# Performance work log

Measured on AMD Instinct MI355X. Metric: run time of the kernel, lower is better.

Reference implementation:

```python
import jax, jax.numpy as jnp
import numpy as np

N, E, D, H = 20000, 320000, 128, 256
NUM_FINE = 2


def _mlp(x, W1, b1, W2, b2):
    # Linear -> relu -> Linear -> relu (dropout rate 0.0 is identity)
    h = jax.nn.relu(x @ W1 + b1)
    return jax.nn.relu(h @ W2 + b2)


def setup_inputs() -> dict:
    key = jax.random.key(0)
    ks = jax.random.split(key, 12)

    def p(k, shape):
        fan_in = shape[0]
        return jax.random.normal(k, shape, jnp.float32) * (1.0 / fan_in) ** 0.5

    return {
        "nodes": jax.random.normal(ks[0], (N, D), jnp.float32),
        "edges": jax.random.normal(ks[1], (E, D), jnp.float32),
        "senders": jax.random.randint(ks[2], (E,), 0, N, jnp.int32),
        "receivers": jax.random.randint(ks[3], (E,), 0, N, jnp.int32),
        # embed node MLP: D -> H -> D
        "Wn1": p(ks[4], (D, H)), "bn1": jnp.zeros((H,), jnp.float32),
        "Wn2": p(ks[5], (H, D)), "bn2": jnp.zeros((D,), jnp.float32),
        # embed edge MLP: D -> H -> D
        "We1": p(ks[6], (D, H)), "be1": jnp.zeros((H,), jnp.float32),
        "We2": p(ks[7], (H, D)), "be2": jnp.zeros((D,), jnp.float32),
        # edge model MLP: 3D -> H -> D  (concat[src, dest, edge_attr])
        "Wed1": p(ks[8], (3 * D, H)), "bed1": jnp.zeros((H,), jnp.float32),
        "Wed2": p(ks[9], (H, D)), "bed2": jnp.zeros((D,), jnp.float32),
        # node model MLP: 2D -> H -> D  (concat[x, segment_sum(edge_attr)])
        "Wnd1": p(ks[10], (2 * D, H)), "bnd1": jnp.zeros((H,), jnp.float32),
        "Wnd2": p(ks[11], (H, D)), "bnd2": jnp.zeros((D,), jnp.float32),
    }


def reference(nodes, edges, senders, receivers,
              Wn1, bn1, Wn2, bn2, We1, be1, We2, be2,
              Wed1, bed1, Wed2, bed2, Wnd1, bnd1, Wnd2, bnd2):
    # Embed stage (EmbedMetaLayer)
    x = _mlp(nodes, Wn1, bn1, Wn2, bn2)   # (N, D)
    e = _mlp(edges, We1, be1, We2, be2)   # (E, D)

    pooled = []
    for _ in range(NUM_FINE):
        # EdgeModel: gather src/dest node feats, concat with edge feats, MLP
        edge_in = jnp.concatenate([x[senders], x[receivers], e], axis=-1)  # (E, 3D)
        e = _mlp(edge_in, Wed1, bed1, Wed2, bed2)                           # (E, D)
        # NodeModel: scatter-add edge feats to receiver nodes, concat, MLP
        agg = jax.ops.segment_sum(e, receivers, num_segments=N)            # (N, D)
        x = _mlp(jnp.concatenate([x, agg], axis=-1), Wnd1, bnd1, Wnd2, bnd2)  # (N, D)
        # global_add_pooling: vmap(jnp.sum) over nodes -> per-node feature sum (N,)
        pooled.append(jnp.sum(x, axis=-1))
    # concatenate along last axis of the 1-D pooled vectors -> (NUM_FINE * N,)
    return jnp.concatenate(pooled, axis=-1)
```

## Files before the change

### kernel.cpp

```cpp
#include <hip/hip_runtime.h>
#include <stdint.h>

#define N_NODES 20000
#define N_EDGES 320000

typedef __attribute__((ext_vector_type(8)))  __bf16        bf16x8;
typedef __attribute__((ext_vector_type(16))) float         f32x16;
typedef __attribute__((ext_vector_type(4)))  float         f32x4v;
typedef __attribute__((ext_vector_type(4)))  uint32_t      u32x4;
typedef __attribute__((ext_vector_type(8)))  unsigned short us8;
typedef __attribute__((ext_vector_type(2)))  unsigned short us2;

static __device__ __forceinline__ unsigned short cvt_bf16(float f) {
  uint32_t u = __builtin_bit_cast(uint32_t, f);
  u = (u + 0x7fffu + ((u >> 16) & 1u)) >> 16;
  return (unsigned short)u;
}
static __device__ __forceinline__ float cvt_f32(unsigned short h) {
  uint32_t u = ((uint32_t)h) << 16;
  return __builtin_bit_cast(float, u);
}

static __device__ __forceinline__ void gll16(const void* g, void* l) {
  __builtin_amdgcn_global_load_lds(
      (const __attribute__((address_space(1))) unsigned int*)g,
      (__attribute__((address_space(3))) unsigned int*)l, 16, 0, 0);
}

#define WAITV(n) do { \
  if ((n) == 0)      asm volatile("s_waitcnt vmcnt(0)" ::: "memory"); \
  else if ((n) == 4) asm volatile("s_waitcnt vmcnt(4)" ::: "memory"); \
  else if ((n) == 8) asm volatile("s_waitcnt vmcnt(8)" ::: "memory"); \
  else               asm volatile("s_waitcnt vmcnt(12)" ::: "memory"); \
} while (0)

__global__ void pack_w(const float* __restrict__ W, unsigned short* __restrict__ out,
                       int K, int Ncols) {
  int idx = blockIdx.x * 256 + threadIdx.x;
  int total = K * Ncols;
  if (idx >= total) return;
  int e    = idx & 7;
  int lane = (idx >> 3) & 63;
  int t    = idx >> 9;
  int ntiles = Ncols >> 5;
  int nt = t % ntiles;
  int ks = t / ntiles;
  int k = ks * 16 + (lane >> 5) * 8 + e;
  int c = nt * 32 + (lane & 31);
  out[idx] = cvt_bf16(W[(size_t)k * Ncols + c]);
}

__global__ void pack_w2(const float* __restrict__ W, unsigned short* __restrict__ out) {
  int idx = blockIdx.x * 256 + threadIdx.x;
  if (idx >= 32768) return;
  int e    = idx & 7;
  int lane = (idx >> 3) & 63;
  int t    = idx >> 9;
  int nt = t & 3, ks = t >> 2;
  int k = ks * 16 + ((lane >> 5) << 2) + (e & 3) + ((e >> 2) << 3);
  int c = nt * 32 + (lane & 31);
  out[idx] = cvt_bf16(W[(size_t)k * 128 + c]);
}

__global__ void hist_k(const int* __restrict__ recv, int* __restrict__ cnt, int n) {
  int i = blockIdx.x * 256 + threadIdx.x;
  if (i < n) atomicAdd(&cnt[recv[i]], 1);
}

__global__ void scan_k(const int* __restrict__ cnt, int* __restrict__ off,
                       int* __restrict__ cursor, int n) {
  __shared__ int part[1024];
  int t = threadIdx.x;
  int chunk = (n + 1023) / 1024;
  int base = t * chunk;
  int s = 0;
  for (int i = 0; i < chunk; ++i) { int idx = base + i; if (idx < n) s += cnt[idx]; }
  part[t] = s;
  __syncthreads();
  for (int d = 1; d < 1024; d <<= 1) {
    int v = (t >= d) ? part[t - d] : 0;
    __syncthreads();
    part[t] += v;
    __syncthreads();
  }
  int prefix = (t > 0) ? part[t - 1] : 0;
  for (int i = 0; i < chunk; ++i) {
    int idx = base + i;
    if (idx < n) { off[idx] = prefix; cursor[idx] = prefix; prefix += cnt[idx]; }
  }
  if (t == 1023) off[n] = part[1023];
}

__global__ void fill_k(const int* __restrict__ recv, int* __restrict__ cursor,
                       int* __restrict__ pos, int n) {
  int i = blockIdx.x * 256 + threadIdx.x;
  if (i < n) {
    int p = atomicAdd(&cursor[recv[i]], 1);
    pos[i] = p;
  }
}

__global__ void agg_k(const unsigned short* __restrict__ eb, const int* __restrict__ off,
                      unsigned short* __restrict__ aggb, int n) {
  int node = blockIdx.x * 4 + (threadIdx.x >> 6);
  if (node >= n) return;
  int lane = threadIdx.x & 63;
  float a0 = 0.f, a1 = 0.f;
  int s = off[node], t = off[node + 1];
  for (int q = s; q < t; ++q) {
    us2 v = *(const us2*)(eb + (size_t)q * 128 + lane * 2);
    a0 += cvt_f32(v[0]);
    a1 += cvt_f32(v[1]);
  }
  us2 r; r[0] = cvt_bf16(a0); r[1] = cvt_bf16(a1);
  *(us2*)(aggb + (size_t)node * 128 + lane * 2) = r;
}

template <int KIN, int MODE, int POOL>
__global__ __launch_bounds__(256, 2)
void mlp_kernel(const float* __restrict__ srcf,
                const unsigned short* __restrict__ xb,
                const unsigned short* __restrict__ ebuf,
                const unsigned short* __restrict__ aggb,
                const int* __restrict__ senders,
                const int* __restrict__ receivers,
                const int* __restrict__ perm,
                const unsigned short* __restrict__ P1,
                const float* __restrict__ b1,
                const unsigned short* __restrict__ P2,
                const float* __restrict__ b2,
                unsigned short* __restrict__ dst,
                float* __restrict__ pool_out,
                int nrows) {
  constexpr int NS1 = KIN / 32;
  constexpr int NP  = NS1 / 2;
  __shared__ __align__(16) unsigned char lds[65536];

  const int tid  = threadIdx.x;
  const int lane = tid & 63;
  const int wid  = tid >> 6;
  const int g    = lane >> 5;
  const int l31  = lane & 31;
  const int rowBlock = blockIdx.x << 7;

  const unsigned char* P1b = (const unsigned char*)P1;
  const unsigned char* P2b = (const unsigned char*)P2;

  int grow = rowBlock + wid * 32 + l31;
  if (grow >= nrows) grow = nrows - 1;

  const unsigned short *pS = nullptr, *pR = nullptr, *pE = nullptr;
  const unsigned short *pX = nullptr, *pAg = nullptr;
  const float* fb = nullptr;
  if constexpr (MODE == 0) {
    fb = srcf + (size_t)grow * KIN;
  } else if constexpr (MODE == 1) {
    pS = xb + (size_t)senders[grow] * 128;
    pR = xb + (size_t)receivers[grow] * 128;
    pE = ebuf + (size_t)perm[grow] * 128;
  } else {
    pX  = xb + (size_t)grow * 128;
    pAg = aggb + (size_t)grow * 128;
  }

  auto STG1 = [&](int s) {
    unsigned char* bW = lds + (s & 3) * 16384;
#pragma unroll
    for (int c = 0; c < 4; ++c)
      gll16(P1b + (size_t)s * 16384 + c * 4096 + tid * 16,
            bW + c * 4096 + wid * 1024);
  };
  auto STG2 = [&](int c) {
    unsigned char* bW = lds + ((c + NS1) & 3) * 16384;
#pragma unroll
    for (int q = 0; q < 4; ++q)
      gll16(P2b + (size_t)c * 16384 + q * 4096 + tid * 16,
            bW + q * 4096 + wid * 1024);
  };

  auto LROW = [&](int s, us8* o) {
    const int k0s = s * 32;
    const unsigned short* p;
    if constexpr (MODE == 1) {
      const int seg = k0s >> 7;
      p = (seg == 0) ? pS : (seg == 1) ? pR : pE;
    } else {
      p = (k0s >> 7) ? pAg : pX;
    }
    const int ko = k0s & 127;
    o[0] = *(const us8*)(p + ko + g * 8);
    o[1] = *(const us8*)(p + ko + 16 + g * 8);
  };
  auto LROWF = [&](int s, f32x4v* rf) {
    const float* p = fb + s * 32 + g * 8;
    rf[0] = *(const f32x4v*)(p);
    rf[1] = *(const f32x4v*)(p + 4);
    rf[2] = *(const f32x4v*)(p + 16);
    rf[3] = *(const f32x4v*)(p + 20);
  };
  auto MKBR = [&](const f32x4v* rf, bf16x8& b0v, bf16x8& b1v) {
    us8 h0, h1;
#pragma unroll
    for (int e = 0; e < 4; ++e) {
      h0[e] = cvt_bf16(rf[0][e]); h0[4 + e] = cvt_bf16(rf[1][e]);
      h1[e] = cvt_bf16(rf[2][e]); h1[4 + e] = cvt_bf16(rf[3][e]);
    }
    b0v = __builtin_bit_cast(bf16x8, h0);
    b1v = __builtin_bit_cast(bf16x8, h1);
  };

  f32x16 acc1[8];
#pragma unroll
  for (int t = 0; t < 8; ++t)
#pragma unroll
    for (int k = 0; k < 16; ++k) acc1[t][k] = 0.0f;

  auto COMPUTE = [&](const unsigned char* bW, bf16x8 b0v, bf16x8 b1v) {
#pragma unroll
    for (int kc = 0; kc < 2; ++kc) {
      const bf16x8 bv = kc ? b1v : b0v;
#pragma unroll
      for (int nt = 0; nt < 8; ++nt) {
        bf16x8 av = __builtin_bit_cast(bf16x8,
            *(const us8*)(bW + (kc * 8 + nt) * 1024 + lane * 16));
        acc1[nt] = __builtin_amdgcn_mfma_f32_32x32x16_bf16(av, bv, acc1[nt], 0, 0, 0);
      }
    }
  };

  us8    rr[4][2];
  f32x4v rf[4][4];

  STG1(0); STG1(1);
  if constexpr (MODE == 0) { LROWF(0, rf[0]); LROWF(1, rf[1]); LROWF(2, rf[2]); LROWF(3, rf[3]); }
  else                     { LROW(0, rr[0]);  LROW(1, rr[1]);  LROW(2, rr[2]);  LROW(3, rr[3]); }

#pragma unroll
  for (int p = 0; p < NP; ++p) {
    const int s0 = 2 * p, s1 = 2 * p + 1;
    const int w = (p + 1 < NP) ? ((MODE == 0) ? 8 : 4) : 0;
    WAITV(w);
    asm volatile("s_waitcnt lgkmcnt(0)" ::: "memory");
    asm volatile("s_barrier" ::: "memory");

    bf16x8 a0v, a1v, c0v, c1v;
    if constexpr (MODE == 0) { MKBR(rf[s0 & 3], a0v, a1v); MKBR(rf[s1 & 3], c0v, c1v); }
    else {
      a0v = __builtin_bit_cast(bf16x8, rr[s0 & 3][0]); a1v = __builtin_bit_cast(bf16x8, rr[s0 & 3][1]);
      c0v = __builtin_bit_cast(bf16x8, rr[s1 & 3][0]); c1v = __builtin_bit_cast(bf16x8, rr[s1 & 3][1]);
    }

    if (p + 1 < NP) {
      STG1(s0 + 2); STG1(s1 + 2);
      if (p + 2 < NP) {
        if constexpr (MODE == 0) { LROWF(s0 + 4, rf[(s0 + 4) & 3]); LROWF(s1 + 4, rf[(s1 + 4) & 3]); }
        else                     { LROW(s0 + 4, rr[(s0 + 4) & 3]);  LROW(s1 + 4, rr[(s1 + 4) & 3]); }
      }
    }

    __builtin_amdgcn_s_setprio(1);
    COMPUTE(lds + (s0 & 3) * 16384, a0v, a1v);
    COMPUTE(lds + (s1 & 3) * 16384, c0v, c1v);
    __builtin_amdgcn_s_setprio(0);
  }

  STG2(0);
  STG2(1);

  u32x4 pa4[16];
#pragma unroll
  for (int t = 0; t < 8; ++t) {
#pragma unroll
    for (int q4 = 0; q4 < 4; ++q4) {
      const f32x4v bv4 = *(const f32x4v*)(b1 + t * 32 + q4 * 8 + g * 4);
      float v0 = fmaxf(acc1[t][q4 * 4 + 0] + bv4[0], 0.0f);
      float v1 = fmaxf(acc1[t][q4 * 4 + 1] + bv4[1], 0.0f);
      float v2 = fmaxf(acc1[t][q4 * 4 + 2] + bv4[2], 0.0f);
      float v3 = fmaxf(acc1[t][q4 * 4 + 3] + bv4[3], 0.0f);
      uint32_t lo, hi;
      asm("v_cvt_pk_bf16_f32 %0, %1, %2" : "=v"(lo) : "v"(v0), "v"(v1));
      asm("v_cvt_pk_bf16_f32 %0, %1, %2" : "=v"(hi) : "v"(v2), "v"(v3));
      pa4[t * 2 + (q4 >> 1)][(q4 & 1) * 2 + 0] = lo;
      pa4[t * 2 + (q4 >> 1)][(q4 & 1) * 2 + 1] = hi;
    }
  }

  f32x16 acc2[4];
#pragma unroll
  for (int nt = 0; nt < 4; ++nt)
#pragma unroll
    for (int k = 0; k < 16; ++k) acc2[nt][k] = 0.0f;

#pragma unroll
  for (int q = 0; q < 2; ++q) {
    WAITV(0);
    asm volatile("s_waitcnt lgkmcnt(0)" ::: "memory");
    asm volatile("s_barrier" ::: "memory");
    if (q == 0) { STG2(2); STG2(3); }
    __builtin_amdgcn_s_setprio(1);
#pragma unroll
    for (int ci = 0; ci < 2; ++ci) {
      const int c = q * 2 + ci;
      const unsigned char* bW = lds + ((c + NS1) & 3) * 16384;
#pragma unroll
      for (int kk = 0; kk < 4; ++kk) {
        const bf16x8 a2 = __builtin_bit_cast(bf16x8, pa4[c * 4 + kk]);
#pragma unroll
        for (int nt = 0; nt < 4; ++nt) {
          const bf16x8 bw = __builtin_bit_cast(bf16x8,
              *(const us8*)(bW + (kk * 4 + nt) * 1024 + lane * 16));
          acc2[nt] = __builtin_amdgcn_mfma_f32_32x32x16_bf16(a2, bw, acc2[nt], 0, 0, 0);
        }
      }
    }
    __builtin_amdgcn_s_setprio(0);
  }

  float bias2[4];
#pragma unroll
  for (int nt = 0; nt < 4; ++nt) bias2[nt] = b2[nt * 32 + l31];

#pragma unroll
  for (int reg = 0; reg < 16; ++reg) {
    const int rowpat = (reg & 3) + ((reg >> 2) << 3) + g * 4;
    const int row = rowBlock + wid * 32 + rowpat;
    const bool ok = (row < nrows);
    size_t drow = 0;
    if (ok) drow = (size_t)((MODE <= 1 && perm) ? perm[row] : row);
    float vs = 0.0f;
#pragma unroll
    for (int nt = 0; nt < 4; ++nt) {
      float v = fmaxf(acc2[nt][reg] + bias2[nt], 0.0f);
      vs += v;
      if (ok) dst[drow * 128 + nt * 32 + l31] = cvt_bf16(v);
    }
    if constexpr (POOL) {
#pragma unroll
      for (int m = 1; m <= 16; m <<= 1) vs += __shfl_xor(vs, m, 64);
      if (l31 == 0 && ok) pool_out[row] = vs;
    }
  }
}

static constexpr size_t OFF_X    = 0;
static constexpr size_t OFF_E    = 5120000;
static constexpr size_t OFF_AGG  = 87040000;
static constexpr size_t OFF_PN1  = 92160000;
static constexpr size_t OFF_PN2  = OFF_PN1 + 65536;
static constexpr size_t OFF_PE1  = OFF_PN2 + 65536;
static constexpr size_t OFF_PE2  = OFF_PE1 + 65536;
static constexpr size_t OFF_PD1  = OFF_PE2 + 65536;
static constexpr size_t OFF_PD2  = OFF_PD1 + 196608;
static constexpr size_t OFF_PM1  = OFF_PD2 + 65536;
static constexpr size_t OFF_PM2  = OFF_PM1 + 131072;
static constexpr size_t OFF_CNT  = OFF_PM2 + 65536;
static constexpr size_t OFF_OFFS = OFF_CNT + 80000;
static constexpr size_t OFF_CUR  = OFF_OFFS + 80004;
static constexpr size_t OFF_POS  = OFF_CUR + 80000;

extern "C" void kernel_launch(void* const* d_in, const int* in_sizes, int n_in,
                              void* d_out, int out_size, void* d_ws, size_t ws_size,
                              hipStream_t stream) {
  const float* nodes = (const float*)d_in[0];
  const float* edges = (const float*)d_in[1];
  const int* senders = (const int*)d_in[2];
  const int* receivers = (const int*)d_in[3];
  const float* Wn1 = (const float*)d_in[4];  const float* bn1 = (const float*)d_in[5];
  const float* Wn2 = (const float*)d_in[6];  const float* bn2 = (const float*)d_in[7];
  const float* We1 = (const float*)d_in[8];  const float* be1 = (const float*)d_in[9];
  const float* We2 = (const float*)d_in[10]; const float* be2 = (const float*)d_in[11];
  const float* Wed1 = (const float*)d_in[12]; const float* bed1 = (const float*)d_in[13];
  const float* Wed2 = (const float*)d_in[14]; const float* bed2 = (const float*)d_in[15];
  const float* Wnd1 = (const float*)d_in[16]; const float* bnd1 = (const float*)d_in[17];
  const float* Wnd2 = (const float*)d_in[18]; const float* bnd2 = (const float*)d_in[19];

  char* ws = (char*)d_ws;
  unsigned short* xb   = (unsigned short*)(ws + OFF_X);
  unsigned short* eb   = (unsigned short*)(ws + OFF_E);
  unsigned short* aggb = (unsigned short*)(ws + OFF_AGG);
  unsigned short* Pn1  = (unsigned short*)(ws + OFF_PN1);
  unsigned short* Pn2  = (unsigned short*)(ws + OFF_PN2);
  unsigned short* Pe1  = (unsigned short*)(ws + OFF_PE1);
  unsigned short* Pe2  = (unsigned short*)(ws + OFF_PE2);
  unsigned short* Pd1  = (unsigned short*)(ws + OFF_PD1);
  unsigned short* Pd2  = (unsigned short*)(ws + OFF_PD2);
  unsigned short* Pm1  = (unsigned short*)(ws + OFF_PM1);
  unsigned short* Pm2  = (unsigned short*)(ws + OFF_PM2);
  int* cnt    = (int*)(ws + OFF_CNT);
  int* offs   = (int*)(ws + OFF_OFFS);
  int* cursor = (int*)(ws + OFF_CUR);
  int* pos    = (int*)(ws + OFF_POS);
  float* outp = (float*)d_out;

  pack_w<<<128, 256, 0, stream>>>(Wn1, Pn1, 128, 256);
  pack_w2<<<128, 256, 0, stream>>>(Wn2, Pn2);
  pack_w<<<128, 256, 0, stream>>>(We1, Pe1, 128, 256);
  pack_w2<<<128, 256, 0, stream>>>(We2, Pe2);
  pack_w<<<384, 256, 0, stream>>>(Wed1, Pd1, 384, 256);
  pack_w2<<<128, 256, 0, stream>>>(Wed2, Pd2);
  pack_w<<<256, 256, 0, stream>>>(Wnd1, Pm1, 256, 256);
  pack_w2<<<128, 256, 0, stream>>>(Wnd2, Pm2);

  hipMemsetAsync(cnt, 0, (size_t)N_NODES * 4, stream);
  hist_k<<<1250, 256, 0, stream>>>(receivers, cnt, N_EDGES);
  scan_k<<<1, 1024, 0, stream>>>(cnt, offs, cursor, N_NODES);
  fill_k<<<1250, 256, 0, stream>>>(receivers, cursor, pos, N_EDGES);

  const int nodeBlocks = (N_NODES + 127) / 128;
  const int edgeBlocks = N_EDGES / 128;

  mlp_kernel<128, 0, 0><<<nodeBlocks, 256, 0, stream>>>(
      nodes, nullptr, nullptr, nullptr, nullptr, nullptr, nullptr,
      Pn1, bn1, Pn2, bn2, xb, nullptr, N_NODES);
  mlp_kernel<128, 0, 0><<<edgeBlocks, 256, 0, stream>>>(
      edges, nullptr, nullptr, nullptr, nullptr, nullptr, pos,
      Pe1, be1, Pe2, be2, eb, nullptr, N_EDGES);

  for (int it = 0; it < 2; ++it) {
    mlp_kernel<384, 1, 0><<<edgeBlocks, 256, 0, stream>>>(
        nullptr, xb, eb, nullptr, senders, receivers, pos,
        Pd1, bed1, Pd2, bed2, eb, nullptr, N_EDGES);
    agg_k<<<(N_NODES + 3) / 4, 256, 0, stream>>>(eb, offs, aggb, N_NODES);
    mlp_kernel<256, 2, 1><<<nodeBlocks, 256, 0, stream>>>(
        nullptr, xb, nullptr, aggb, nullptr, nullptr, nullptr,
        Pm1, bnd1, Pm2, bnd2, xb, outp + (size_t)it * N_NODES, N_NODES);
  }
}
```

Baseline: 497.7 us.

## Precompute per-node projections of edge MLP first layer and gather them

Splits the edge MLP first layer so the sender and receiver blocks of Wed1 are applied once per node (20k rows) in a new precompute kernel, storing bf16 partial products per node. The edge kernel then runs only a K=128 GEMM on edge features and adds the gathered sender/receiver partial sums, and edges are kept in receiver-sorted order using new sorted sender/receiver index arrays. This cuts the edge-side first-layer FLOPs by about two thirds but adds a 1 KB-per-edge gather of precomputed projections and an extra bf16 rounding of the partial sums.

```diff
diff --git a/kernel.cpp b/kernel.cpp
--- a/kernel.cpp
+++ b/kernel.cpp
@@ -28,10 +28,12 @@
 }
 
 #define WAITV(n) do { \
-  if ((n) == 0)      asm volatile("s_waitcnt vmcnt(0)" ::: "memory"); \
-  else if ((n) == 4) asm volatile("s_waitcnt vmcnt(4)" ::: "memory"); \
-  else if ((n) == 8) asm volatile("s_waitcnt vmcnt(8)" ::: "memory"); \
-  else               asm volatile("s_waitcnt vmcnt(12)" ::: "memory"); \
+  if ((n) == 0)       asm volatile("s_waitcnt vmcnt(0)"  ::: "memory"); \
+  else if ((n) == 4)  asm volatile("s_waitcnt vmcnt(4)"  ::: "memory"); \
+  else if ((n) == 8)  asm volatile("s_waitcnt vmcnt(8)"  ::: "memory"); \
+  else if ((n) == 12) asm volatile("s_waitcnt vmcnt(12)" ::: "memory"); \
+  else if ((n) == 16) asm volatile("s_waitcnt vmcnt(16)" ::: "memory"); \
+  else                asm volatile("s_waitcnt vmcnt(24)" ::: "memory"); \
 } while (0)
 
 __global__ void pack_w(const float* __restrict__ W, unsigned short* __restrict__ out,
@@ -91,12 +93,15 @@
   if (t == 1023) off[n] = part[1023];
 }
 
-__global__ void fill_k(const int* __restrict__ recv, int* __restrict__ cursor,
-                       int* __restrict__ pos, int n) {
+__global__ void fill_k(const int* __restrict__ send, const int* __restrict__ recv,
+                       int* __restrict__ cursor, int* __restrict__ pos,
+                       int* __restrict__ ssend, int* __restrict__ srecv, int n) {
   int i = blockIdx.x * 256 + threadIdx.x;
   if (i < n) {
     int p = atomicAdd(&cursor[recv[i]], 1);
     pos[i] = p;
+    ssend[p] = send[i];
+    srecv[p] = recv[i];
   }
 }
 
@@ -116,12 +121,91 @@
   *(us2*)(aggb + (size_t)node * 128 + lane * 2) = r;
 }
 
+__global__ __launch_bounds__(256, 2)
+void precompute_k(const unsigned short* __restrict__ xb,
+                  const unsigned short* __restrict__ Pd1,
+                  unsigned short* __restrict__ XP, int nrows) {
+  __shared__ __align__(16) unsigned char lds[65536];
+  const int tid = threadIdx.x, lane = tid & 63, wid = tid >> 6;
+  const int g = lane >> 5, l31 = lane & 31;
+  const int rowBlock = blockIdx.x << 7;
+  int grow = rowBlock + wid * 32 + l31;
+  if (grow >= nrows) grow = nrows - 1;
+  const unsigned short* pX = xb + (size_t)grow * 128;
+  const unsigned char* Pb = (const unsigned char*)Pd1;
+
+  auto STG = [&](int s, int buf) {
+    unsigned char* bW = lds + buf * 16384;
+#pragma unroll
+    for (int c = 0; c < 4; ++c)
+      gll16(Pb + (size_t)s * 16384 + c * 4096 + tid * 16, bW + c * 4096 + wid * 1024);
+  };
+
+  us8 rows[4][2];
+#pragma unroll
+  for (int s = 0; s < 4; ++s) {
+    rows[s][0] = *(const us8*)(pX + s * 32 + g * 8);
+    rows[s][1] = *(const us8*)(pX + s * 32 + 16 + g * 8);
+  }
+  STG(0, 0); STG(1, 1); STG(2, 2); STG(3, 3);
+
+  f32x16 acc[8];
+  auto ZERO = [&]() {
+#pragma unroll
+    for (int t = 0; t < 8; ++t)
+#pragma unroll
+      for (int k = 0; k < 16; ++k) acc[t][k] = 0.0f;
+  };
+  auto COMP = [&](int buf, bf16x8 b0v, bf16x8 b1v) {
+    const unsigned char* bW = lds + buf * 16384;
+#pragma unroll
+    for (int kc = 0; kc < 2; ++kc) {
+      const bf16x8 bv = kc ? b1v : b0v;
+#pragma unroll
+      for (int nt = 0; nt < 8; ++nt) {
+        bf16x8 av = __builtin_bit_cast(bf16x8,
+            *(const us8*)(bW + (kc * 8 + nt) * 1024 + lane * 16));
+        acc[nt] = __builtin_amdgcn_mfma_f32_32x32x16_bf16(av, bv, acc[nt], 0, 0, 0);
+      }
+    }
+  };
+  auto WOUT = [&](int m) {
+    unsigned short* dst = XP + (((size_t)grow * 2 + m) * 2 + g) * 128;
+#pragma unroll
+    for (int t = 0; t < 8; ++t) {
+      us8 h0, h1;
+#pragma unroll
+      for (int j = 0; j < 8; ++j) { h0[j] = cvt_bf16(acc[t][j]); h1[j] = cvt_bf16(acc[t][8 + j]); }
+      *(us8*)(dst + t * 16) = h0;
+      *(us8*)(dst + t * 16 + 8) = h1;
+    }
+  };
+
+  ZERO();
+  WAITV(0);
+  asm volatile("s_barrier" ::: "memory");
+#pragma unroll
+  for (int s = 0; s < 4; ++s)
+    COMP(s, __builtin_bit_cast(bf16x8, rows[s][0]), __builtin_bit_cast(bf16x8, rows[s][1]));
+  asm volatile("s_waitcnt lgkmcnt(0)" ::: "memory");
+  asm volatile("s_barrier" ::: "memory");
+  STG(4, 0); STG(5, 1); STG(6, 2); STG(7, 3);
+  WOUT(0);
+  ZERO();
+  WAITV(0);
+  asm volatile("s_barrier" ::: "memory");
+#pragma unroll
+  for (int s = 0; s < 4; ++s)
+    COMP(s, __builtin_bit_cast(bf16x8, rows[s][0]), __builtin_bit_cast(bf16x8, rows[s][1]));
+  WOUT(1);
+}
+
 template <int KIN, int MODE, int POOL>
 __global__ __launch_bounds__(256, 2)
 void mlp_kernel(const float* __restrict__ srcf,
                 const unsigned short* __restrict__ xb,
                 const unsigned short* __restrict__ ebuf,
-                const unsigned short* __restrict__ aggb,
+                const unsigned short* __restrict__ xpb,
                 const int* __restrict__ senders,
                 const int* __restrict__ receivers,
                 const int* __restrict__ perm,
@@ -149,18 +233,18 @@
   int grow = rowBlock + wid * 32 + l31;
   if (grow >= nrows) grow = nrows - 1;
 
-  const unsigned short *pS = nullptr, *pR = nullptr, *pE = nullptr;
-  const unsigned short *pX = nullptr, *pAg = nullptr;
+  const unsigned short *pE = nullptr, *pX = nullptr, *pAg = nullptr;
+  const unsigned short *pXa = nullptr, *pXb = nullptr;
   const float* fb = nullptr;
   if constexpr (MODE == 0) {
     fb = srcf + (size_t)grow * KIN;
   } else if constexpr (MODE == 1) {
-    pS = xb + (size_t)senders[grow] * 128;
-    pR = xb + (size_t)receivers[grow] * 128;
-    pE = ebuf + (size_t)perm[grow] * 128;
+    pE  = ebuf + (size_t)grow * 128;
+    pXa = xpb + (size_t)senders[grow] * 512 + g * 128;
+    pXb = xpb + (size_t)receivers[grow] * 512 + 256 + g * 128;
   } else {
     pX  = xb + (size_t)grow * 128;
-    pAg = aggb + (size_t)grow * 128;
+    pAg = xpb + (size_t)grow * 128;
   }
 
   auto STG1 = [&](int s) {
@@ -179,15 +263,10 @@
   };
 
   auto LROW = [&](int s, us8* o) {
-    const int k0s = s * 32;
     const unsigned short* p;
-    if constexpr (MODE == 1) {
-      const int seg = k0s >> 7;
-      p = (seg == 0) ? pS : (seg == 1) ? pR : pE;
-    } else {
-      p = (k0s >> 7) ? pAg : pX;
-    }
-    const int ko = k0s & 127;
+    int ko;
+    if constexpr (MODE == 1) { p = pE; ko = s * 32; }
+    else { const int k0s = s * 32; p = (k0s >> 7) ? pAg : pX; ko = k0s & 127; }
     o[0] = *(const us8*)(p + ko + g * 8);
     o[1] = *(const us8*)(p + ko + 16 + g * 8);
   };
@@ -230,42 +309,98 @@
 
   us8    rr[4][2];
   f32x4v rf[4][4];
-
-  STG1(0); STG1(1);
-  if constexpr (MODE == 0) { LROWF(0, rf[0]); LROWF(1, rf[1]); LROWF(2, rf[2]); LROWF(3, rf[3]); }
-  else                     { LROW(0, rr[0]);  LROW(1, rr[1]);  LROW(2, rr[2]);  LROW(3, rr[3]); }
-
-#pragma unroll
-  for (int p = 0; p < NP; ++p) {
-    const int s0 = 2 * p, s1 = 2 * p + 1;
-    const int w = (p + 1 < NP) ? ((MODE == 0) ? 8 : 4) : 0;
-    WAITV(w);
+  us8    xps[2][8];
+
+  auto XPLOAD = [&](int k, int slot) {
+    us8* d = xps[slot];
+#pragma unroll
+    for (int tt = 0; tt < 2; ++tt) {
+      const int t = 2 * k + tt;
+      d[tt * 2 + 0]     = *(const us8*)(pXa + t * 16);
+      d[tt * 2 + 1]     = *(const us8*)(pXa + t * 16 + 8);
+      d[4 + tt * 2 + 0] = *(const us8*)(pXb + t * 16);
+      d[4 + tt * 2 + 1] = *(const us8*)(pXb + t * 16 + 8);
+    }
+  };
+  auto XPFOLD = [&](int k, int slot) {
+    const us8* d = xps[slot];
+#pragma unroll
+    for (int tt = 0; tt < 2; ++tt) {
+      const int t = 2 * k + tt;
+#pragma unroll
+      for (int j = 0; j < 16; ++j) {
+        acc1[t][j] += cvt_f32(d[tt * 2 + (j >> 3)][j & 7]) +
+                      cvt_f32(d[4 + tt * 2 + (j >> 3)][j & 7]);
+      }
+    }
+  };
+
+  if constexpr (MODE == 1) {
+    STG1(0); STG1(1); STG1(2); STG1(3);
+    LROW(0, rr[0]); LROW(1, rr[1]); LROW(2, rr[2]); LROW(3, rr[3]);
+    WAITV(4);
     asm volatile("s_waitcnt lgkmcnt(0)" ::: "memory");
     asm volatile("s_barrier" ::: "memory");
-
-    bf16x8 a0v, a1v, c0v, c1v;
-    if constexpr (MODE == 0) { MKBR(rf[s0 & 3], a0v, a1v); MKBR(rf[s1 & 3], c0v, c1v); }
-    else {
-      a0v = __builtin_bit_cast(bf16x8, rr[s0 & 3][0]); a1v = __builtin_bit_cast(bf16x8, rr[s0 & 3][1]);
-      c0v = __builtin_bit_cast(bf16x8, rr[s1 & 3][0]); c1v = __builtin_bit_cast(bf16x8, rr[s1 & 3][1]);
-    }
-
-    if (p + 1 < NP) {
-      STG1(s0 + 2); STG1(s1 + 2);
-      if (p + 2 < NP) {
-        if constexpr (MODE == 0) { LROWF(s0 + 4, rf[(s0 + 4) & 3]); LROWF(s1 + 4, rf[(s1 + 4) & 3]); }
-        else                     { LROW(s0 + 4, rr[(s0 + 4) & 3]);  LROW(s1 + 4, rr[(s1 + 4) & 3]); }
+    {
+      bf16x8 a0 = __builtin_bit_cast(bf16x8, rr[0][0]), a1 = __builtin_bit_cast(bf16x8, rr[0][1]);
+      bf16x8 a2 = __builtin_bit_cast(bf16x8, rr[1][0]), a3 = __builtin_bit_cast(bf16x8, rr[1][1]);
+      XPLOAD(0, 0); XPLOAD(1, 1);
+      __builtin_amdgcn_s_setprio(1);
+      COMPUTE(lds, a0, a1);
+      COMPUTE(lds + 16384, a2, a3);
+      __builtin_amdgcn_s_setprio(0);
+    }
+    WAITV(16);
+    {
+      bf16x8 a0 = __builtin_bit_cast(bf16x8, rr[2][0]), a1 = __builtin_bit_cast(bf16x8, rr[2][1]);
+      bf16x8 a2 = __builtin_bit_cast(bf16x8, rr[3][0]), a3 = __builtin_bit_cast(bf16x8, rr[3][1]);
+      __builtin_amdgcn_s_setprio(1);
+      COMPUTE(lds + 2 * 16384, a0, a1);
+      COMPUTE(lds + 3 * 16384, a2, a3);
+      __builtin_amdgcn_s_setprio(0);
+    }
+    asm volatile("s_waitcnt lgkmcnt(0)" ::: "memory");
+    asm volatile("s_barrier" ::: "memory");
+    STG2(0); STG2(1);
+    WAITV(16);  XPFOLD(0, 0);
+    XPLOAD(2, 0);
+    WAITV(16);  XPFOLD(1, 1);
+    XPLOAD(3, 1);
+    WAITV(8);   XPFOLD(2, 0);
+    WAITV(0);   XPFOLD(3, 1);
+  } else {
+    STG1(0); STG1(1);
+    if constexpr (MODE == 0) { LROWF(0, rf[0]); LROWF(1, rf[1]); LROWF(2, rf[2]); LROWF(3, rf[3]); }
+    else                     { LROW(0, rr[0]);  LROW(1, rr[1]);  LROW(2, rr[2]);  LROW(3, rr[3]); }
+
+#pragma unroll
+    for (int p = 0; p < NP; ++p) {
+      const int s0 = 2 * p, s1 = 2 * p + 1;
+      const int w = (p + 1 < NP) ? ((MODE == 0) ? 8 : 4) : 0;
+      WAITV(w);
+      asm volatile("s_waitcnt lgkmcnt(0)" ::: "memory");
+      asm volatile("s_barrier" ::: "memory");
+
+      bf16x8 a0v, a1v, c0v, c1v;
+      if constexpr (MODE == 0) { MKBR(rf[s0 & 3], a0v, a1v); MKBR(rf[s1 & 3], c0v, c1v); }
+      else {
+        a0v = __builtin_bit_cast(bf16x8, rr[s0 & 3][0]); a1v = __builtin_bit_cast(bf16x8, rr[s0 & 3][1]);
+        c0v = __builtin_bit_cast(bf16x8, rr[s1 & 3][0]); c1v = __builtin_bit_cast(bf16x8, rr[s1 & 3][1]);
       }
-    }
-
-    __builtin_amdgcn_s_setprio(1);
-    COMPUTE(lds + (s0 & 3) * 16384, a0v, a1v);
-    COMPUTE(lds + (s1 & 3) * 16384, c0v, c1v);
-    __builtin_amdgcn_s_setprio(0);
-  }
-
-  STG2(0);
-  STG2(1);
+      if (p + 1 < NP) {
+        STG1(s0 + 2); STG1(s1 + 2);
+        if (p + 2 < NP) {
+          if constexpr (MODE == 0) { LROWF(s0 + 4, rf[(s0 + 4) & 3]); LROWF(s1 + 4, rf[(s1 + 4) & 3]); }
+          else                     { LROW(s0 + 4, rr[(s0 + 4) & 3]);  LROW(s1 + 4, rr[(s1 + 4) & 3]); }
+        }
+      }
+      __builtin_amdgcn_s_setprio(1);
+      COMPUTE(lds + (s0 & 3) * 16384, a0v, a1v);
+      COMPUTE(lds + (s1 & 3) * 16384, c0v, c1v);
+      __builtin_amdgcn_s_setprio(0);
+    }
+    STG2(0); STG2(1);
+  }
 
   u32x4 pa4[16];
 #pragma unroll
@@ -326,7 +461,7 @@
     const int row = rowBlock + wid * 32 + rowpat;
     const bool ok = (row < nrows);
     size_t drow = 0;
-    if (ok) drow = (size_t)((MODE <= 1 && perm) ? perm[row] : row);
+    if (ok) drow = (size_t)((MODE == 0 && perm) ? perm[row] : row);
     float vs = 0.0f;
 #pragma unroll
     for (int nt = 0; nt < 4; ++nt) {
@@ -357,6 +492,9 @@
 static constexpr size_t OFF_OFFS = OFF_CNT + 80000;
 static constexpr size_t OFF_CUR  = OFF_OFFS + 80004;
 static constexpr size_t OFF_POS  = OFF_CUR + 80000;
+static constexpr size_t OFF_SSEND= OFF_POS + 1280000;
+static constexpr size_t OFF_SREC = OFF_SSEND + 1280000;
+static constexpr size_t OFF_XP   = ((OFF_SREC + 1280000 + 63) / 64) * 64;
 
 extern "C" void kernel_launch(void* const* d_in, const int* in_sizes, int n_in,
                               void* d_out, int out_size, void* d_ws, size_t ws_size,
@@ -390,6 +528,9 @@
   int* offs   = (int*)(ws + OFF_OFFS);
   int* cursor = (int*)(ws + OFF_CUR);
   int* pos    = (int*)(ws + OFF_POS);
+  int* ssend  = (int*)(ws + OFF_SSEND);
+  int* srecv  = (int*)(ws + OFF_SREC);
+  unsigned short* XP = (unsigned short*)(ws + OFF_XP);
   float* outp = (float*)d_out;
 
   pack_w<<<128, 256, 0, stream>>>(Wn1, Pn1, 128, 256);
@@ -404,7 +545,7 @@
   hipMemsetAsync(cnt, 0, (size_t)N_NODES * 4, stream);
   hist_k<<<1250, 256, 0, stream>>>(receivers, cnt, N_EDGES);
   scan_k<<<1, 1024, 0, stream>>>(cnt, offs, cursor, N_NODES);
-  fill_k<<<1250, 256, 0, stream>>>(receivers, cursor, pos, N_EDGES);
+  fill_k<<<1250, 256, 0, stream>>>(senders, receivers, cursor, pos, ssend, srecv, N_EDGES);
 
   const int nodeBlocks = (N_NODES + 127) / 128;
   const int edgeBlocks = N_EDGES / 128;
@@ -417,9 +558,10 @@
       Pe1, be1, Pe2, be2, eb, nullptr, N_EDGES);
 
   for (int it = 0; it < 2; ++it) {
-    mlp_kernel<384, 1, 0><<<edgeBlocks, 256, 0, stream>>>(
-        nullptr, xb, eb, nullptr, senders, receivers, pos,
-        Pd1, bed1, Pd2, bed2, eb, nullptr, N_EDGES);
+    precompute_k<<<nodeBlocks, 256, 0, stream>>>(xb, Pd1, XP, N_NODES);
+    mlp_kernel<128, 1, 0><<<edgeBlocks, 256, 0, stream>>>(
+        nullptr, nullptr, eb, XP, ssend, srecv, nullptr,
+        Pd1 + 8 * 8192, bed1, Pd2, bed2, eb, nullptr, N_EDGES);
     agg_k<<<(N_NODES + 3) / 4, 256, 0, stream>>>(eb, offs, aggb, N_NODES);
     mlp_kernel<256, 2, 1><<<nodeBlocks, 256, 0, stream>>>(
         nullptr, xb, nullptr, aggb, nullptr, nullptr, nullptr,
```

After: 504.7 us. No clear change (+1.4%).

## Process edges in receiver-sorted order and merge weight packing into one launch

Applied to the files above, without the earlier changes.

fill_k now scatters senders and receivers into receiver-sorted arrays, so the edge-model kernel reads and writes edge features contiguously in sorted order instead of going through the perm indirection. Receiver-row gathers also become clustered, which should improve cache locality, and the permuted edge-feature reads and writes become coalesced. The eight weight-packing launches are merged into a single pack_all kernel to cut launch overhead. The cost is two extra 1.28 MB scatter writes per call in fill_k.

```diff
diff --git a/kernel.cpp b/kernel.cpp
--- a/kernel.cpp
+++ b/kernel.cpp
@@ -34,11 +34,9 @@
   else               asm volatile("s_waitcnt vmcnt(12)" ::: "memory"); \
 } while (0)
 
-__global__ void pack_w(const float* __restrict__ W, unsigned short* __restrict__ out,
-                       int K, int Ncols) {
-  int idx = blockIdx.x * 256 + threadIdx.x;
-  int total = K * Ncols;
-  if (idx >= total) return;
+static __device__ __forceinline__ void pw_body(const float* __restrict__ W,
+                                               unsigned short* __restrict__ out,
+                                               int Ncols, int idx) {
   int e    = idx & 7;
   int lane = (idx >> 3) & 63;
   int t    = idx >> 9;
@@ -49,10 +47,9 @@
   int c = nt * 32 + (lane & 31);
   out[idx] = cvt_bf16(W[(size_t)k * Ncols + c]);
 }
-
-__global__ void pack_w2(const float* __restrict__ W, unsigned short* __restrict__ out) {
-  int idx = blockIdx.x * 256 + threadIdx.x;
-  if (idx >= 32768) return;
+static __device__ __forceinline__ void pw2_body(const float* __restrict__ W,
+                                                unsigned short* __restrict__ out,
+                                                int idx) {
   int e    = idx & 7;
   int lane = (idx >> 3) & 63;
   int t    = idx >> 9;
@@ -60,6 +57,25 @@
   int k = ks * 16 + ((lane >> 5) << 2) + (e & 3) + ((e >> 2) << 3);
   int c = nt * 32 + (lane & 31);
   out[idx] = cvt_bf16(W[(size_t)k * 128 + c]);
+}
+
+__global__ void pack_all(const float* __restrict__ Wn1, const float* __restrict__ Wn2,
+                         const float* __restrict__ We1, const float* __restrict__ We2,
+                         const float* __restrict__ Wed1, const float* __restrict__ Wed2,
+                         const float* __restrict__ Wnd1, const float* __restrict__ Wnd2,
+                         unsigned short* __restrict__ Pn1, unsigned short* __restrict__ Pn2,
+                         unsigned short* __restrict__ Pe1, unsigned short* __restrict__ Pe2,
+                         unsigned short* __restrict__ Pd1, unsigned short* __restrict__ Pd2,
+                         unsigned short* __restrict__ Pm1, unsigned short* __restrict__ Pm2) {
+  const int b = blockIdx.x, tid = threadIdx.x;
+  if      (b <  128) pw_body(Wn1,  Pn1, 256, (b        ) * 256 + tid);
+  else if (b <  256) pw_body(We1,  Pe1, 256, (b -  128) * 256 + tid);
+  else if (b <  640) pw_body(Wed1, Pd1, 256, (b -  256) * 256 + tid);
+  else if (b <  896) pw_body(Wnd1, Pm1, 256, (b -  640) * 256 + tid);
+  else if (b < 1024) pw2_body(Wn2,  Pn2, (b -  896) * 256 + tid);
+  else if (b < 1152) pw2_body(We2,  Pe2, (b - 1024) * 256 + tid);
+  else if (b < 1280) pw2_body(Wed2, Pd2, (b - 1152) * 256 + tid);
+  else               pw2_body(Wnd2, Pm2, (b - 1280) * 256 + tid);
 }
 
 __global__ void hist_k(const int* __restrict__ recv, int* __restrict__ cnt, int n) {
@@ -91,12 +107,15 @@
   if (t == 1023) off[n] = part[1023];
 }
 
-__global__ void fill_k(const int* __restrict__ recv, int* __restrict__ cursor,
-                       int* __restrict__ pos, int n) {
+__global__ void fill_k(const int* __restrict__ send, const int* __restrict__ recv,
+                       int* __restrict__ cursor, int* __restrict__ pos,
+                       int* __restrict__ ssend, int* __restrict__ srecv, int n) {
   int i = blockIdx.x * 256 + threadIdx.x;
   if (i < n) {
     int p = atomicAdd(&cursor[recv[i]], 1);
     pos[i] = p;
+    ssend[p] = send[i];
+    srecv[p] = recv[i];
   }
 }
 
@@ -157,7 +176,7 @@
   } else if constexpr (MODE == 1) {
     pS = xb + (size_t)senders[grow] * 128;
     pR = xb + (size_t)receivers[grow] * 128;
-    pE = ebuf + (size_t)perm[grow] * 128;
+    pE = ebuf + (size_t)grow * 128;
   } else {
     pX  = xb + (size_t)grow * 128;
     pAg = aggb + (size_t)grow * 128;
@@ -326,7 +345,7 @@
     const int row = rowBlock + wid * 32 + rowpat;
     const bool ok = (row < nrows);
     size_t drow = 0;
-    if (ok) drow = (size_t)((MODE <= 1 && perm) ? perm[row] : row);
+    if (ok) drow = (size_t)((MODE == 0 && perm) ? perm[row] : row);
     float vs = 0.0f;
 #pragma unroll
     for (int nt = 0; nt < 4; ++nt) {
@@ -357,6 +376,8 @@
 static constexpr size_t OFF_OFFS = OFF_CNT + 80000;
 static constexpr size_t OFF_CUR  = OFF_OFFS + 80004;
 static constexpr size_t OFF_POS  = OFF_CUR + 80000;
+static constexpr size_t OFF_SSEND= OFF_POS + 1280000;
+static constexpr size_t OFF_SREC = OFF_SSEND + 1280000;
 
 extern "C" void kernel_launch(void* const* d_in, const int* in_sizes, int n_in,
                               void* d_out, int out_size, void* d_ws, size_t ws_size,
@@ -390,21 +411,17 @@
   int* offs   = (int*)(ws + OFF_OFFS);
   int* cursor = (int*)(ws + OFF_CUR);
   int* pos    = (int*)(ws + OFF_POS);
+  int* ssend  = (int*)(ws + OFF_SSEND);
+  int* srecv  = (int*)(ws + OFF_SREC);
   float* outp = (float*)d_out;
 
-  pack_w<<<128, 256, 0, stream>>>(Wn1, Pn1, 128, 256);
-  pack_w2<<<128, 256, 0, stream>>>(Wn2, Pn2);
-  pack_w<<<128, 256, 0, stream>>>(We1, Pe1, 128, 256);
-  pack_w2<<<128, 256, 0, stream>>>(We2, Pe2);
-  pack_w<<<384, 256, 0, stream>>>(Wed1, Pd1, 384, 256);
-  pack_w2<<<128, 256, 0, stream>>>(Wed2, Pd2);
-  pack_w<<<256, 256, 0, stream>>>(Wnd1, Pm1, 256, 256);
-  pack_w2<<<128, 256, 0, stream>>>(Wnd2, Pm2);
+  pack_all<<<1408, 256, 0, stream>>>(Wn1, Wn2, We1, We2, Wed1, Wed2, Wnd1, Wnd2,
+                                     Pn1, Pn2, Pe1, Pe2, Pd1, Pd2, Pm1, Pm2);
 
   hipMemsetAsync(cnt, 0, (size_t)N_NODES * 4, stream);
   hist_k<<<1250, 256, 0, stream>>>(receivers, cnt, N_EDGES);
   scan_k<<<1, 1024, 0, stream>>>(cnt, offs, cursor, N_NODES);
-  fill_k<<<1250, 256, 0, stream>>>(receivers, cursor, pos, N_EDGES);
+  fill_k<<<1250, 256, 0, stream>>>(senders, receivers, cursor, pos, ssend, srecv, N_EDGES);
 
   const int nodeBlocks = (N_NODES + 127) / 128;
   const int edgeBlocks = N_EDGES / 128;
@@ -418,7 +435,7 @@
 
   for (int it = 0; it < 2; ++it) {
     mlp_kernel<384, 1, 0><<<edgeBlocks, 256, 0, stream>>>(
-        nullptr, xb, eb, nullptr, senders, receivers, pos,
+        nullptr, xb, eb, nullptr, ssend, srecv, nullptr,
         Pd1, bed1, Pd2, bed2, eb, nullptr, N_EDGES);
     agg_k<<<(N_NODES + 3) / 4, 256, 0, stream>>>(eb, offs, aggb, N_NODES);
     mlp_kernel<256, 2, 1><<<nodeBlocks, 256, 0, stream>>>(
```

After: 479.6 us. 1.04x faster.
